# Optimization experiments

Hardware: AMD Instinct MI355X
Metric: run time of the kernel (lower is better)

The kernel has to match this reference:

```python
import jax, jax.numpy as jnp
import numpy as np


def setup_inputs() -> dict:
    N, E, F, H, C = 50000, 400000, 256, 256, 64
    key = jax.random.key(0)
    ks = jax.random.split(key, 6)
    s = 1.0 / np.sqrt(F)
    return {
        "x": jax.random.normal(ks[0], (N, F), dtype=jnp.float32),
        "edge_index": jax.random.randint(ks[1], (2, E), 0, N, dtype=jnp.int64),
        "W1": jax.random.normal(ks[2], (F, H), dtype=jnp.float32) * s,
        "b1": jnp.zeros((H,), dtype=jnp.float32),
        "W2": jax.random.normal(ks[3], (H, H), dtype=jnp.float32) * s,
        "b2": jnp.zeros((H,), dtype=jnp.float32),
        "Wh": jax.random.normal(ks[4], (H, C), dtype=jnp.float32) * s,
        "bh": jnp.zeros((C,), dtype=jnp.float32),
    }


def _gcn_layer(x, row, col, norm, W, b, n_nodes):
    # linear first (PyG GCNLayer: x = self.linear(x) before propagate)
    h = x @ W + b                      # [N, H]
    msg = norm[:, None] * h[row]       # x_j = x[source]; scale by sym norm
    return jax.ops.segment_sum(msg, col, num_segments=n_nodes)  # aggr='add' at target


def reference(x, edge_index, W1, b1, W2, b2, Wh, bh):
    N = x.shape[0]
    # add self loops
    loops = jnp.arange(N, dtype=edge_index.dtype)
    row = jnp.concatenate([edge_index[0], loops])  # source
    col = jnp.concatenate([edge_index[1], loops])  # target
    # degree via scatter_add of ones on row (as in source)
    deg = jax.ops.segment_sum(jnp.ones(row.shape[0], dtype=x.dtype), row, num_segments=N)
    deg_inv_sqrt = jnp.where(deg > 0, jax.lax.rsqrt(jnp.maximum(deg, 1.0)), 0.0)
    norm = deg_inv_sqrt[row] * deg_inv_sqrt[col]
    # two GCN layers with ReLU (dropout inactive in eval mode)
    h = jax.nn.relu(_gcn_layer(x, row, col, norm, W1, b1, N))
    h = jax.nn.relu(_gcn_layer(h, row, col, norm, W2, b2, N))
    # vertex task: no pooling, just head
    return h @ Wh + bh
```

## Files before the change

kernel.cpp:

```cpp
#include <hip/hip_runtime.h>
#include <hip/hip_bf16.h>

typedef __attribute__((ext_vector_type(8))) short short8;
typedef __attribute__((ext_vector_type(4))) float f32x4;

static inline int cdiv(int a, int b) { return (a + b - 1) / b; }

__device__ inline float bf2f(unsigned short u) {
    union { unsigned int u; float f; } a; a.u = ((unsigned int)u) << 16; return a.f;
}
__device__ inline unsigned short f2bf(float f) {
    union { float f; unsigned int u; } a; a.f = f;
    unsigned int r = a.u + 0x7fff + ((a.u >> 16) & 1);
    return (unsigned short)(r >> 16);
}
__device__ inline void gload_lds16(const void* g, void* l) {
    __builtin_amdgcn_global_load_lds(
        (const __attribute__((address_space(1))) unsigned int*)g,
        (__attribute__((address_space(3))) unsigned int*)l, 16, 0, 0);
}

__global__ __launch_bounds__(256) void count_both_k(
    const int* __restrict__ rows, const int* __restrict__ cols,
    float* deg, int* indeg, int E)
{
    int e = blockIdx.x * 256 + threadIdx.x;
    if (e < E) {
        atomicAdd(&deg[rows[e]], 1.0f);
        atomicAdd(&indeg[cols[e]], 1);
    }
}

__global__ __launch_bounds__(256) void scan_block_k(
    const int* __restrict__ indeg, int* __restrict__ rowstart, int* __restrict__ bsums, int N)
{
    __shared__ int smem[256];
    int b = blockIdx.x, t = threadIdx.x;
    int base = b * 1024 + t * 4;
    int v0 = (base + 0 < N) ? indeg[base + 0] : 0;
    int v1 = (base + 1 < N) ? indeg[base + 1] : 0;
    int v2 = (base + 2 < N) ? indeg[base + 2] : 0;
    int v3 = (base + 3 < N) ? indeg[base + 3] : 0;
    int s = v0 + v1 + v2 + v3;
    smem[t] = s;
    __syncthreads();
    for (int off = 1; off < 256; off <<= 1) {
        int x = smem[t];
        int y = (t >= off) ? smem[t - off] : 0;
        __syncthreads();
        smem[t] = x + y;
        __syncthreads();
    }
    int excl = smem[t] - s;
    if (base + 0 < N) rowstart[base + 0] = excl;
    if (base + 1 < N) rowstart[base + 1] = excl + v0;
    if (base + 2 < N) rowstart[base + 2] = excl + v0 + v1;
    if (base + 3 < N) rowstart[base + 3] = excl + v0 + v1 + v2;
    if (t == 255) bsums[b] = smem[255];
}

__global__ __launch_bounds__(256) void scan_add_dinv_k(
    int* rowstart, int* cursor, const int* __restrict__ bsums, int nb,
    float* deg, int N, int E)
{
    __shared__ int sb[64];
    int t = threadIdx.x;
    int v = 0;
    if (t < 64) {
        v = (t < nb) ? bsums[t] : 0;
        sb[t] = v;
    }
    __syncthreads();
    for (int off = 1; off < 64; off <<= 1) {
        int x = 0, y = 0;
        if (t < 64) { x = sb[t]; y = (t >= off) ? sb[t - off] : 0; }
        __syncthreads();
        if (t < 64) sb[t] = x + y;
        __syncthreads();
    }
    if (t < 64) sb[t] -= v;
    __syncthreads();

    int i = blockIdx.x * 256 + t;
    if (i < N) {
        int r = rowstart[i] + sb[i >> 10];
        rowstart[i] = r;
        cursor[i] = r;
        deg[i] = rsqrtf(deg[i] + 1.0f);
    }
    if (blockIdx.x == 0 && t == 0) rowstart[N] = E;
}

__global__ __launch_bounds__(256) void fill_csr_k(
    const int* __restrict__ rows, const int* __restrict__ cols,
    int* cursor, int* __restrict__ csr, int E)
{
    int e = blockIdx.x * 256 + threadIdx.x;
    if (e < E) {
        int pos = atomicAdd(&cursor[cols[e]], 1);
        csr[pos] = rows[e];
    }
}

__global__ __launch_bounds__(256) void prep_weights_zero_k(
    const float* __restrict__ W1, const float* __restrict__ W2, const float* __restrict__ Wh,
    unsigned short* __restrict__ Wt1, unsigned short* __restrict__ Wt2, unsigned short* __restrict__ Wht,
    float4* __restrict__ zp, int nz4)
{
    int idx = blockIdx.x * 256 + threadIdx.x;
    if (idx < nz4) zp[idx] = make_float4(0.f, 0.f, 0.f, 0.f);
    if (idx < 65536) {
        int k = idx >> 8, m = idx & 255;
        Wt1[m * 256 + k] = f2bf(W1[idx]);
    } else if (idx < 131072) {
        int i = idx - 65536;
        int k = i >> 8, m = i & 255;
        Wt2[m * 256 + k] = f2bf(W2[i]);
    } else if (idx < 147456) {
        int i = idx - 131072;
        int k = i >> 6, m = i & 63;
        Wht[m * 256 + k] = f2bf(Wh[i]);
    }
}

template<int BN, int MODE, int ASRC, int NYB>
__global__ __launch_bounds__(256) void gemm_mfma_k(
    const void* __restrict__ Asrc, const unsigned short* __restrict__ Wt,
    const float* __restrict__ bias, const float* __restrict__ rowscale,
    void* __restrict__ Cout, int N, int K, int Ncols)
{
    constexpr int NF = BN / 32;
    __shared__ __align__(16) unsigned short As[2][128 * 64];
    __shared__ __align__(16) unsigned short Bs[2][BN * 64];

    const unsigned short* Ab = (const unsigned short*)Asrc;
    const float* Af = (const float*)Asrc;

    int bx, by;
    if constexpr (NYB == 2) {
        const int nXB = (N + 127) >> 7;
        int d = blockIdx.x;
        int xcd = d & 7, slot = d >> 3;
        by = slot & 1;
        bx = xcd + 8 * (slot >> 1);
        if (bx >= nXB) return;
    } else {
        bx = blockIdx.x; by = 0;
    }

    const int tid = threadIdx.x;
    const int wid = tid >> 6;
    const int lane = tid & 63;
    const int wr = wid >> 1;
    const int wc = wid & 1;
    const int rowBase = bx * 128;
    const int colBase = by * BN;

    f32x4 acc[4][NF];
    #pragma unroll
    for (int m = 0; m < 4; ++m)
        #pragma unroll
        for (int n = 0; n < NF; ++n)
            acc[m][n] = (f32x4)0.0f;

    const int sslot = (lane & 7) ^ (lane >> 3);

    float4 areg[4][2];

    auto stageA_g = [&](int buf, int k0) {
        #pragma unroll
        for (int it = 0; it < 4; ++it) {
            int ch = wid * 4 + it;
            int r = ch * 8 + (lane >> 3);
            int grow = rowBase + r; if (grow >= N) grow = N - 1;
            gload_lds16(Ab + (size_t)grow * K + k0 + sslot * 8, (void*)&As[buf][ch * 512]);
        }
    };
    auto issueA = [&](int k0) {
        #pragma unroll
        for (int it = 0; it < 4; ++it) {
            int ch = wid * 4 + it;
            int r = ch * 8 + (lane >> 3);
            int grow = rowBase + r; if (grow >= N) grow = N - 1;
            const float* src = Af + (size_t)grow * K + k0 + sslot * 8;
            areg[it][0] = *(const float4*)src;
            areg[it][1] = *(const float4*)(src + 4);
        }
    };
    auto writeA = [&](int buf) {
        #pragma unroll
        for (int it = 0; it < 4; ++it) {
            int ch = wid * 4 + it;
            short8 w;
            w[0] = (short)f2bf(areg[it][0].x); w[1] = (short)f2bf(areg[it][0].y);
            w[2] = (short)f2bf(areg[it][0].z); w[3] = (short)f2bf(areg[it][0].w);
            w[4] = (short)f2bf(areg[it][1].x); w[5] = (short)f2bf(areg[it][1].y);
            w[6] = (short)f2bf(areg[it][1].z); w[7] = (short)f2bf(areg[it][1].w);
            *(short8*)&As[buf][ch * 512 + lane * 8] = w;
        }
    };
    auto stageB = [&](int buf, int k0) {
        #pragma unroll
        for (int it = 0; it < NF; ++it) {
            int ch = wid * NF + it;
            int c = ch * 8 + (lane >> 3);
            gload_lds16(Wt + (size_t)(colBase + c) * K + k0 + sslot * 8, (void*)&Bs[buf][ch * 512]);
        }
    };

    const int nt = K >> 6;
    if constexpr (ASRC == 0) {
        stageA_g(0, 0);
        stageB(0, 0);
    } else {
        issueA(0);
        stageB(0, 0);
        writeA(0);
    }
    __syncthreads();

    int cur = 0;
    for (int t = 0; t < nt; ++t) {
        if (t + 1 < nt) {
            if constexpr (ASRC == 0) stageA_g(cur ^ 1, (t + 1) * 64);
            else issueA((t + 1) * 64);
            stageB(cur ^ 1, (t + 1) * 64);
        }
        #pragma unroll
        for (int ks = 0; ks < 2; ++ks) {
            short8 af[4];
            #pragma unroll
            for (int m = 0; m < 4; ++m) {
                int R = wr * 64 + m * 16 + (lane & 15);
                int p = (ks * 4 + (lane >> 4)) ^ (R & 7);
                af[m] = *(const short8*)(&As[cur][R * 64 + p * 8]);
            }
            #pragma unroll
            for (int n = 0; n < NF; ++n) {
                int Cc = wc * (BN / 2) + n * 16 + (lane & 15);
                int p = (ks * 4 + (lane >> 4)) ^ (Cc & 7);
                short8 bf = *(const short8*)(&Bs[cur][Cc * 64 + p * 8]);
                #pragma unroll
                for (int m = 0; m < 4; ++m)
                    acc[m][n] = __builtin_amdgcn_mfma_f32_16x16x32_bf16(af[m], bf, acc[m][n], 0, 0, 0);
            }
        }
        if (t + 1 < nt) {
            if constexpr (ASRC == 1) writeA(cur ^ 1);
            __syncthreads();
        }
        cur ^= 1;
    }

    float bv[NF];
    int colv[NF];
    #pragma unroll
    for (int n = 0; n < NF; ++n) {
        colv[n] = colBase + wc * (BN / 2) + n * 16 + (lane & 15);
        bv[n] = bias[colv[n]];
    }
    #pragma unroll
    for (int m = 0; m < 4; ++m) {
        #pragma unroll
        for (int q = 0; q < 4; ++q) {
            int row = rowBase + wr * 64 + m * 16 + (lane >> 4) * 4 + q;
            if (row >= N) continue;
            if (MODE == 0) {
                float sc = rowscale[row];
                unsigned short* Cb = (unsigned short*)Cout;
                #pragma unroll
                for (int n = 0; n < NF; ++n)
                    Cb[(size_t)row * Ncols + colv[n]] = f2bf((acc[m][n][q] + bv[n]) * sc);
            } else {
                float* Cf = (float*)Cout;
                #pragma unroll
                for (int n = 0; n < NF; ++n)
                    Cf[(size_t)row * Ncols + colv[n]] = acc[m][n][q] + bv[n];
            }
        }
    }
}

__global__ __launch_bounds__(256) void gather_agg_k(
    const int* __restrict__ rowstart, const int* __restrict__ csr,
    const float* __restrict__ dinv, const unsigned short* __restrict__ hp,
    unsigned short* __restrict__ out, int N)
{
    int c = __builtin_amdgcn_readfirstlane(blockIdx.x * 4 + (threadIdx.x >> 6));
    if (c >= N) return;
    int lane = threadIdx.x & 63;
    const ushort4* base = (const ushort4*)hp;
    int beg = rowstart[c], end = rowstart[c + 1];

    ushort4 sv = base[(size_t)c * 64 + lane];
    float a0 = bf2f(sv.x), a1 = bf2f(sv.y), a2 = bf2f(sv.z), a3 = bf2f(sv.w);

    int e = beg;
    for (; e + 8 <= end; e += 8) {
        ushort4 v0 = base[(size_t)csr[e + 0] * 64 + lane];
        ushort4 v1 = base[(size_t)csr[e + 1] * 64 + lane];
        ushort4 v2 = base[(size_t)csr[e + 2] * 64 + lane];
        ushort4 v3 = base[(size_t)csr[e + 3] * 64 + lane];
        ushort4 v4 = base[(size_t)csr[e + 4] * 64 + lane];
        ushort4 v5 = base[(size_t)csr[e + 5] * 64 + lane];
        ushort4 v6 = base[(size_t)csr[e + 6] * 64 + lane];
        ushort4 v7 = base[(size_t)csr[e + 7] * 64 + lane];
        a0 += bf2f(v0.x) + bf2f(v1.x) + bf2f(v2.x) + bf2f(v3.x)
            + bf2f(v4.x) + bf2f(v5.x) + bf2f(v6.x) + bf2f(v7.x);
        a1 += bf2f(v0.y) + bf2f(v1.y) + bf2f(v2.y) + bf2f(v3.y)
            + bf2f(v4.y) + bf2f(v5.y) + bf2f(v6.y) + bf2f(v7.y);
        a2 += bf2f(v0.z) + bf2f(v1.z) + bf2f(v2.z) + bf2f(v3.z)
            + bf2f(v4.z) + bf2f(v5.z) + bf2f(v6.z) + bf2f(v7.z);
        a3 += bf2f(v0.w) + bf2f(v1.w) + bf2f(v2.w) + bf2f(v3.w)
            + bf2f(v4.w) + bf2f(v5.w) + bf2f(v6.w) + bf2f(v7.w);
    }
    for (; e + 4 <= end; e += 4) {
        ushort4 v0 = base[(size_t)csr[e + 0] * 64 + lane];
        ushort4 v1 = base[(size_t)csr[e + 1] * 64 + lane];
        ushort4 v2 = base[(size_t)csr[e + 2] * 64 + lane];
        ushort4 v3 = base[(size_t)csr[e + 3] * 64 + lane];
        a0 += bf2f(v0.x) + bf2f(v1.x) + bf2f(v2.x) + bf2f(v3.x);
        a1 += bf2f(v0.y) + bf2f(v1.y) + bf2f(v2.y) + bf2f(v3.y);
        a2 += bf2f(v0.z) + bf2f(v1.z) + bf2f(v2.z) + bf2f(v3.z);
        a3 += bf2f(v0.w) + bf2f(v1.w) + bf2f(v2.w) + bf2f(v3.w);
    }
    for (; e < end; ++e) {
        ushort4 v0 = base[(size_t)csr[e] * 64 + lane];
        a0 += bf2f(v0.x); a1 += bf2f(v0.y); a2 += bf2f(v0.z); a3 += bf2f(v0.w);
    }

    float sc = dinv[c];
    ushort4 o;
    o.x = f2bf(fmaxf(sc * a0, 0.f));
    o.y = f2bf(fmaxf(sc * a1, 0.f));
    o.z = f2bf(fmaxf(sc * a2, 0.f));
    o.w = f2bf(fmaxf(sc * a3, 0.f));
    ((ushort4*)out)[(size_t)c * 64 + lane] = o;
}

extern "C" void kernel_launch(void* const* d_in, const int* in_sizes, int n_in,
                              void* d_out, int out_size, void* d_ws, size_t ws_size,
                              hipStream_t stream) {
    const float* x  = (const float*)d_in[0];
    const int*  ei  = (const int*)d_in[1];
    const float* W1 = (const float*)d_in[2];
    const float* b1 = (const float*)d_in[3];
    const float* W2 = (const float*)d_in[4];
    const float* b2 = (const float*)d_in[5];
    const float* Wh = (const float*)d_in[6];
    const float* bh = (const float*)d_in[7];
    float* out = (float*)d_out;

    const int N = in_sizes[0] / 256;
    const int E = in_sizes[1] / 2;
    const int H = 256;
    const int C = 64;
    const int* rows = ei;
    const int* cols = ei + E;

    char* ws = (char*)d_ws;
    size_t off = 0;
    auto alloc = [&](size_t bytes) {
        void* p = ws + off;
        off = (off + bytes + 255) & ~(size_t)255;
        return p;
    };
    float* deg      = (float*)alloc((size_t)2 * N * 4);
    int*   indeg    = (int*)(deg + N);
    int*   rowstart = (int*)alloc((size_t)(N + 1) * 4);
    int*   bsums    = (int*)alloc(256 * 4);
    int*   csr      = (int*)alloc((size_t)E * 4);
    unsigned short* bufH = (unsigned short*)alloc((size_t)N * H * 2);
    unsigned short* bufA = (unsigned short*)alloc((size_t)N * H * 2);
    unsigned short* Wt1  = (unsigned short*)alloc((size_t)H * H * 2);
    unsigned short* Wt2  = (unsigned short*)alloc((size_t)H * H * 2);
    unsigned short* Wht  = (unsigned short*)alloc((size_t)C * H * 2);

    const int nb = cdiv(N, 1024);

    prep_weights_zero_k<<<cdiv(147456, 256), 256, 0, stream>>>(
        W1, W2, Wh, Wt1, Wt2, Wht, (float4*)deg, 2 * N / 4);
    count_both_k<<<cdiv(E, 256), 256, 0, stream>>>(rows, cols, deg, indeg, E);
    scan_block_k<<<nb, 256, 0, stream>>>(indeg, rowstart, bsums, N);
    scan_add_dinv_k<<<cdiv(N, 256), 256, 0, stream>>>(rowstart, indeg, bsums, nb, deg, N, E);
    fill_csr_k<<<cdiv(E, 256), 256, 0, stream>>>(rows, cols, indeg, csr, E);
    float* dinv = deg;

    const int nXB = cdiv(N, 128);
    dim3 g1(16 * cdiv(nXB, 8));
    dim3 gh(nXB);

    gemm_mfma_k<128, 0, 1, 2><<<g1, 256, 0, stream>>>(x, Wt1, b1, dinv, bufH, N, H, H);
    gather_agg_k<<<cdiv(N, 4), 256, 0, stream>>>(rowstart, csr, dinv, bufH, bufA, N);

    gemm_mfma_k<128, 0, 0, 2><<<g1, 256, 0, stream>>>(bufA, Wt2, b2, dinv, bufH, N, H, H);
    gather_agg_k<<<cdiv(N, 4), 256, 0, stream>>>(rowstart, csr, dinv, bufH, bufA, N);

    gemm_mfma_k<64, 1, 0, 1><<<gh, 256, 0, stream>>>(bufA, Wht, bh, nullptr, out, N, H, C);
}
```

Before: 198.9 us.

## Replicate degree and cursor counters eightfold to spread atomic contention

Degree counting and CSR fill now use eight replicated counter arrays, chosen by block index, instead of a single array. The scan is rewritten to combine the replicas per node and give each replica its own cursor range. The aim is to reduce atomic contention and serialization on hot addresses. In exchange it costs more memory traffic for zeroing and scanning 8N-sized arrays, plus a larger second-level scan.

```diff
diff --git a/kernel.cpp b/kernel.cpp
--- a/kernel.cpp
+++ b/kernel.cpp
@@ -22,26 +22,32 @@
 
 __global__ __launch_bounds__(256) void count_both_k(
     const int* __restrict__ rows, const int* __restrict__ cols,
-    float* deg, int* indeg, int E)
-{
+    float* deg8, int* indeg8, int E, int N)
+{
+    int rep = blockIdx.x & 7;
     int e = blockIdx.x * 256 + threadIdx.x;
     if (e < E) {
-        atomicAdd(&deg[rows[e]], 1.0f);
-        atomicAdd(&indeg[cols[e]], 1);
+        atomicAdd(&deg8[rep * N + rows[e]], 1.0f);
+        atomicAdd(&indeg8[rep * N + cols[e]], 1);
     }
 }
 
 __global__ __launch_bounds__(256) void scan_block_k(
-    const int* __restrict__ indeg, int* __restrict__ rowstart, int* __restrict__ bsums, int N)
+    const int* __restrict__ indeg8, int* __restrict__ rowstart,
+    int* __restrict__ cursor8, int* __restrict__ bsums, int N)
 {
     __shared__ int smem[256];
     int b = blockIdx.x, t = threadIdx.x;
-    int base = b * 1024 + t * 4;
-    int v0 = (base + 0 < N) ? indeg[base + 0] : 0;
-    int v1 = (base + 1 < N) ? indeg[base + 1] : 0;
-    int v2 = (base + 2 < N) ? indeg[base + 2] : 0;
-    int v3 = (base + 3 < N) ? indeg[base + 3] : 0;
-    int s = v0 + v1 + v2 + v3;
+    int node = b * 128 + (t >> 1);
+    int half = t & 1;
+    int v[4];
+    int s = 0;
+    #pragma unroll
+    for (int j = 0; j < 4; ++j) {
+        int rep = half * 4 + j;
+        v[j] = (node < N) ? indeg8[rep * N + node] : 0;
+        s += v[j];
+    }
     smem[t] = s;
     __syncthreads();
     for (int off = 1; off < 256; off <<= 1) {
@@ -52,52 +58,59 @@
         __syncthreads();
     }
     int excl = smem[t] - s;
-    if (base + 0 < N) rowstart[base + 0] = excl;
-    if (base + 1 < N) rowstart[base + 1] = excl + v0;
-    if (base + 2 < N) rowstart[base + 2] = excl + v0 + v1;
-    if (base + 3 < N) rowstart[base + 3] = excl + v0 + v1 + v2;
+    if (node < N) {
+        int p = excl;
+        #pragma unroll
+        for (int j = 0; j < 4; ++j) {
+            int rep = half * 4 + j;
+            cursor8[rep * N + node] = p;
+            p += v[j];
+        }
+        if (half == 0) rowstart[node] = excl;
+    }
     if (t == 255) bsums[b] = smem[255];
 }
 
 __global__ __launch_bounds__(256) void scan_add_dinv_k(
-    int* rowstart, int* cursor, const int* __restrict__ bsums, int nb,
-    float* deg, int N, int E)
-{
-    __shared__ int sb[64];
+    int* rowstart, int* cursor8, const int* __restrict__ bsums, int nbk,
+    const float* __restrict__ deg8, float* __restrict__ dinv, int N, int E)
+{
+    __shared__ int sb[512];
     int t = threadIdx.x;
-    int v = 0;
-    if (t < 64) {
-        v = (t < nb) ? bsums[t] : 0;
-        sb[t] = v;
-    }
+    sb[t]       = (t < nbk) ? bsums[t] : 0;
+    sb[t + 256] = (t + 256 < nbk) ? bsums[t + 256] : 0;
     __syncthreads();
-    for (int off = 1; off < 64; off <<= 1) {
-        int x = 0, y = 0;
-        if (t < 64) { x = sb[t]; y = (t >= off) ? sb[t - off] : 0; }
+    for (int off = 1; off < 512; off <<= 1) {
+        int x0 = sb[t]       + ((t >= off) ? sb[t - off] : 0);
+        int x1 = sb[t + 256] + ((t + 256 >= off) ? sb[t + 256 - off] : 0);
         __syncthreads();
-        if (t < 64) sb[t] = x + y;
+        sb[t] = x0; sb[t + 256] = x1;
         __syncthreads();
     }
-    if (t < 64) sb[t] -= v;
-    __syncthreads();
-
     int i = blockIdx.x * 256 + t;
     if (i < N) {
-        int r = rowstart[i] + sb[i >> 10];
-        rowstart[i] = r;
-        cursor[i] = r;
-        deg[i] = rsqrtf(deg[i] + 1.0f);
+        int blk = i >> 7;
+        int off = (blk == 0) ? 0 : sb[blk - 1];
+        rowstart[i] += off;
+        float d = 1.0f;
+        #pragma unroll
+        for (int rep = 0; rep < 8; ++rep) {
+            cursor8[rep * N + i] += off;
+            d += deg8[rep * N + i];
+        }
+        dinv[i] = rsqrtf(d);
     }
     if (blockIdx.x == 0 && t == 0) rowstart[N] = E;
 }
 
 __global__ __launch_bounds__(256) void fill_csr_k(
     const int* __restrict__ rows, const int* __restrict__ cols,
-    int* cursor, int* __restrict__ csr, int E)
-{
+    int* cursor8, int* __restrict__ csr, int E, int N)
+{
+    int rep = blockIdx.x & 7;
     int e = blockIdx.x * 256 + threadIdx.x;
     if (e < E) {
-        int pos = atomicAdd(&cursor[cols[e]], 1);
+        int pos = atomicAdd(&cursor8[rep * N + cols[e]], 1);
         csr[pos] = rows[e];
     }
 }
@@ -365,10 +378,12 @@
         off = (off + bytes + 255) & ~(size_t)255;
         return p;
     };
-    float* deg      = (float*)alloc((size_t)2 * N * 4);
-    int*   indeg    = (int*)(deg + N);
+    float* deg8     = (float*)alloc((size_t)8 * N * 4);
+    int*   indeg8   = (int*)alloc((size_t)8 * N * 4);
+    int*   cursor8  = (int*)alloc((size_t)8 * N * 4);
     int*   rowstart = (int*)alloc((size_t)(N + 1) * 4);
-    int*   bsums    = (int*)alloc(256 * 4);
+    int*   bsums    = (int*)alloc(512 * 4);
+    float* dinv     = (float*)alloc((size_t)N * 4);
     int*   csr      = (int*)alloc((size_t)E * 4);
     unsigned short* bufH = (unsigned short*)alloc((size_t)N * H * 2);
     unsigned short* bufA = (unsigned short*)alloc((size_t)N * H * 2);
@@ -376,15 +391,16 @@
     unsigned short* Wt2  = (unsigned short*)alloc((size_t)H * H * 2);
     unsigned short* Wht  = (unsigned short*)alloc((size_t)C * H * 2);
 
-    const int nb = cdiv(N, 1024);
-
-    prep_weights_zero_k<<<cdiv(147456, 256), 256, 0, stream>>>(
-        W1, W2, Wh, Wt1, Wt2, Wht, (float4*)deg, 2 * N / 4);
-    count_both_k<<<cdiv(E, 256), 256, 0, stream>>>(rows, cols, deg, indeg, E);
-    scan_block_k<<<nb, 256, 0, stream>>>(indeg, rowstart, bsums, N);
-    scan_add_dinv_k<<<cdiv(N, 256), 256, 0, stream>>>(rowstart, indeg, bsums, nb, deg, N, E);
-    fill_csr_k<<<cdiv(E, 256), 256, 0, stream>>>(rows, cols, indeg, csr, E);
-    float* dinv = deg;
+    const int nbk = cdiv(N, 128);
+
+    const int nz4 = 4 * N;
+    prep_weights_zero_k<<<cdiv(nz4, 256), 256, 0, stream>>>(
+        W1, W2, Wh, Wt1, Wt2, Wht, (float4*)deg8, nz4);
+    count_both_k<<<cdiv(E, 256), 256, 0, stream>>>(rows, cols, deg8, indeg8, E, N);
+    scan_block_k<<<nbk, 256, 0, stream>>>(indeg8, rowstart, cursor8, bsums, N);
+    scan_add_dinv_k<<<cdiv(N, 256), 256, 0, stream>>>(
+        rowstart, cursor8, bsums, nbk, deg8, dinv, N, E);
+    fill_csr_k<<<cdiv(E, 256), 256, 0, stream>>>(rows, cols, cursor8, csr, E, N);
 
     const int nXB = cdiv(N, 128);
     dim3 g1(16 * cdiv(nXB, 8));
```

Result: no change. 199.3 us (+0.2%).
